# Kernel optimization log

Hardware: AMD Instinct MI355X
Metric: run time of the kernel (lower is better)

## Reference

```python
import jax, jax.numpy as jnp
import numpy as np

N_NODES = 10000
N_EDGES = 640000
F_IN = 128
F_HID = 128
BN_EPS = 1e-5


def _spectral_norm_weight(W, u):
    # One power iteration, matching torch.nn.utils.spectral_norm defaults.
    v = W.T @ u
    v = v / (jnp.linalg.norm(v) + 1e-12)
    u_new = W @ v
    u_new = u_new / (jnp.linalg.norm(u_new) + 1e-12)
    sigma = u_new @ (W @ v)
    return W / sigma


def setup_inputs() -> dict:
    key = jax.random.key(0)
    ks = jax.random.split(key, 8)
    x = jax.random.normal(ks[0], (N_NODES, F_IN), dtype=jnp.float32)
    edge_index = jax.random.randint(ks[1], (2, N_EDGES), 0, N_NODES, dtype=jnp.int64)
    W1 = jax.random.normal(ks[2], (F_HID, F_IN), dtype=jnp.float32) * (1.0 / np.sqrt(F_IN))
    b1 = jax.random.normal(ks[3], (F_HID,), dtype=jnp.float32) * 0.01
    u1 = jax.random.normal(ks[4], (F_HID,), dtype=jnp.float32)
    gamma = jnp.ones((F_HID,), dtype=jnp.float32)
    beta = jnp.zeros((F_HID,), dtype=jnp.float32)
    W2 = jax.random.normal(ks[5], (F_HID, F_HID), dtype=jnp.float32) * (1.0 / np.sqrt(F_HID))
    b2 = jax.random.normal(ks[6], (F_HID,), dtype=jnp.float32) * 0.01
    u2 = jax.random.normal(ks[7], (F_HID,), dtype=jnp.float32)
    return {"x": x, "edge_index": edge_index, "W1": W1, "b1": b1, "u1": u1,
            "gamma": gamma, "beta": beta, "W2": W2, "b2": b2, "u2": u2}


def reference(x, edge_index, W1, b1, u1, gamma, beta, W2, b2, u2):
    src, dst = edge_index[0], edge_index[1]
    # GINConv sum aggregation: out_i = sum_{j in N(i)} x_j
    agg = jax.ops.segment_sum(x[src], dst, num_segments=N_NODES)
    h = x + agg  # eps = 0 (default, train_eps=False)
    # MLP: SN-Linear -> ReLU -> BatchNorm1d (training stats) -> SN-Linear
    h = h @ _spectral_norm_weight(W1, u1).T + b1
    h = jax.nn.relu(h)
    mu = jnp.mean(h, axis=0)
    var = jnp.mean((h - mu) ** 2, axis=0)  # biased var, as torch BN forward
    h = gamma * (h - mu) / jnp.sqrt(var + BN_EPS) + beta
    h = h @ _spectral_norm_weight(W2, u2).T + b2
    return h
```

## Files before the change

kernel.cpp:

```cpp
#include <hip/hip_runtime.h>

#define NF 128
#define FB 128
#define CB 64
#define BPB 128
#define MAXNODE 10240

__device__ __forceinline__ unsigned short f2bf(float f) {
    unsigned int u = __float_as_uint(f);
    unsigned int r = u + 0x7FFFu + ((u >> 16) & 1u);
    return (unsigned short)(r >> 16);
}

__global__ __launch_bounds__(512) void power_hist_kernel(
    const float* __restrict__ W1, const float* __restrict__ u1,
    const float* __restrict__ W2, const float* __restrict__ u2,
    const int* __restrict__ dst, int n_edges,
    int* __restrict__ hist2d, int nbin,
    const float* __restrict__ x, unsigned short* __restrict__ xb, int n_x4,
    float* __restrict__ inv_sigma, float* __restrict__ W1t,
    float* __restrict__ colzero, int* __restrict__ cnts) {
    __shared__ float Wl[128][129];
    __shared__ float us[128], vv[128], part[4][128], red[128];
    __shared__ int hist[MAXNODE];
    int tid = threadIdx.x;

    if (blockIdx.x >= 2 + FB) {
        int cb = blockIdx.x - 2 - FB;
        const float4* x4 = (const float4*)x;
        ushort4* xb4 = (ushort4*)xb;
        for (int i = cb * 512 + tid; i < n_x4; i += CB * 512) {
            float4 v = x4[i];
            ushort4 o;
            o.x = f2bf(v.x); o.y = f2bf(v.y); o.z = f2bf(v.z); o.w = f2bf(v.w);
            xb4[i] = o;
        }
        return;
    }
    if (blockIdx.x >= 2) {
        int fb = blockIdx.x - 2;
        for (int i = tid; i < nbin; i += 512) hist[i] = 0;
        __syncthreads();
        int chunk = (n_edges + FB - 1) / FB;
        int e0 = fb * chunk, e1 = min(e0 + chunk, n_edges);
        int a0 = min(e1, (e0 + 3) & ~3);
        for (int e = e0 + tid; e < a0; e += 512) atomicAdd(&hist[dst[e]], 1);
        const int4* d4 = (const int4*)dst;
        int vs = a0 >> 2, ve = e1 >> 2;
        for (int i = vs + tid; i < ve; i += 512) {
            int4 d = d4[i];
            atomicAdd(&hist[d.x], 1);
            atomicAdd(&hist[d.y], 1);
            atomicAdd(&hist[d.z], 1);
            atomicAdd(&hist[d.w], 1);
        }
        for (int e = (ve << 2) + tid; e < e1; e += 512)
            if (e >= a0) atomicAdd(&hist[dst[e]], 1);
        __syncthreads();
        for (int i = tid; i < nbin; i += 512) hist2d[(size_t)fb * nbin + i] = hist[i];
        return;
    }

    const float* W = blockIdx.x ? W2 : W1;
    const float* u = blockIdx.x ? u2 : u1;
    const float4* W4 = (const float4*)W;
    for (int j = tid; j < 4096; j += 512) {
        float4 w = W4[j];
        int r = j >> 5, c0 = (j & 31) << 2;
        Wl[r][c0] = w.x; Wl[r][c0 + 1] = w.y; Wl[r][c0 + 2] = w.z; Wl[r][c0 + 3] = w.w;
    }
    if (tid < 128) us[tid] = u[tid];
    if (blockIdx.x == 0 && tid >= 256 && tid < 512) colzero[tid - 256] = 0.f;
    if (blockIdx.x == 0 && tid < 2) cnts[tid] = 0;
    __syncthreads();

    int c = tid & 127, sl = tid >> 7;
    float acc = 0.f;
#pragma unroll
    for (int j = 0; j < 32; ++j) acc = fmaf(Wl[sl * 32 + j][c], us[sl * 32 + j], acc);
    part[sl][c] = acc;
    __syncthreads();
    if (tid < 128) {
        float v = part[0][tid] + part[1][tid] + part[2][tid] + part[3][tid];
        vv[tid] = v;
        red[tid] = v * v;
    }
    __syncthreads();
    for (int s = 64; s > 0; s >>= 1) { if (tid < s) red[tid] += red[tid + s]; __syncthreads(); }
    float nv = sqrtf(red[0]) + 1e-12f;
    __syncthreads();
    if (tid < 128) vv[tid] = vv[tid] / nv;
    __syncthreads();

    float t = 0.f;
#pragma unroll
    for (int k = 0; k < 32; ++k) t = fmaf(Wl[c][sl * 32 + k], vv[sl * 32 + k], t);
    part[sl][c] = t;
    __syncthreads();
    if (tid < 128) {
        float tv = part[0][tid] + part[1][tid] + part[2][tid] + part[3][tid];
        red[tid] = tv * tv;
    }
    __syncthreads();
    for (int s = 64; s > 0; s >>= 1) { if (tid < s) red[tid] += red[tid + s]; __syncthreads(); }
    float tt = red[0];
    float is = (sqrtf(tt) + 1e-12f) / tt;
    if (tid == 0) inv_sigma[blockIdx.x] = is;
    if (blockIdx.x == 0) {
        for (int idx = tid; idx < 16384; idx += 512) {
            int k = idx >> 7, j = idx & 127;
            W1t[idx] = Wl[j][k] * is;
        }
    }
}

__global__ __launch_bounds__(512) void scanAB_kernel(int* __restrict__ hist2d,
                                                     int* __restrict__ binOff,
                                                     int nbin, int* __restrict__ cnt) {
    __shared__ int part[4][132];
    __shared__ int sbuf[MAXNODE];
    __shared__ int wsum2[8], wexcl2[8];
    __shared__ int isLast;
    int tid = threadIdx.x;
    int binrel = tid >> 2;
    int q = tid & 3;
    int bin = blockIdx.x * BPB + binrel;
    int fb0 = q * 32;

    int v[32];
    if (bin < nbin) {
#pragma unroll
        for (int f = 0; f < 32; ++f)
            v[f] = hist2d[(size_t)(fb0 + f) * nbin + bin];
        int partial = 0;
#pragma unroll
        for (int f = 0; f < 32; ++f) partial += v[f];
        part[q][binrel] = partial;
    }
    __syncthreads();
    if (bin < nbin) {
        int run = 0;
#pragma unroll
        for (int t = 0; t < 4; ++t)
            if (t < q) run += part[t][binrel];
#pragma unroll
        for (int f = 0; f < 32; ++f) {
            hist2d[(size_t)(fb0 + f) * nbin + bin] = run;
            run += v[f];
        }
        if (q == 3)
            binOff[bin] = part[0][binrel] + part[1][binrel] + part[2][binrel] + part[3][binrel];
    }

    __threadfence();
    __syncthreads();
    if (tid == 0) isLast = (atomicAdd(cnt, 1) == (int)gridDim.x - 1);
    __syncthreads();
    if (!isLast) return;
    __threadfence();

    for (int i = tid; i < nbin; i += 512) sbuf[i] = binOff[i];
    __syncthreads();
    int C = (nbin + 511) >> 9;
    int b0 = tid * C, b1 = min(b0 + C, nbin);
    int ssum = 0;
    for (int i = b0; i < b1; ++i) ssum += sbuf[i];
    int lane = tid & 63, wv = tid >> 6;
    int inc = ssum;
    for (int off = 1; off < 64; off <<= 1) {
        int t = __shfl_up(inc, off);
        if (lane >= off) inc += t;
    }
    if (lane == 63) wsum2[wv] = inc;
    __syncthreads();
    if (tid < 8) {
        int e2 = 0;
        for (int t = 0; t < 8; ++t)
            if (t < tid) e2 += wsum2[t];
        wexcl2[tid] = e2;
    }
    __syncthreads();
    int base = inc - ssum + wexcl2[wv];
    int run2 = base;
    for (int i = b0; i < b1; ++i) {
        int vv2 = sbuf[i];
        sbuf[i] = run2;
        run2 += vv2;
    }
    __syncthreads();
    for (int i = tid; i < nbin; i += 512) binOff[i] = sbuf[i];
    if (tid == 511) binOff[nbin] = wexcl2[7] + wsum2[7];
}

__global__ __launch_bounds__(512) void fill_kernel(
    const int* __restrict__ src, const int* __restrict__ dst,
    const int* __restrict__ hist2d, const int* __restrict__ binOff,
    int* __restrict__ bucket, int nbin, int n_edges) {
    __shared__ int cur[MAXNODE];
    int tid = threadIdx.x, fb = blockIdx.x;
    for (int i = tid; i < nbin; i += 512)
        cur[i] = hist2d[(size_t)fb * nbin + i] + binOff[i];
    __syncthreads();
    int chunk = (n_edges + FB - 1) / FB;
    int e0 = fb * chunk, e1 = min(e0 + chunk, n_edges);
    int a0 = min(e1, (e0 + 3) & ~3);
    for (int e = e0 + tid; e < a0; e += 512) {
        int pos = atomicAdd(&cur[dst[e]], 1);
        bucket[pos] = src[e];
    }
    const int4* d4 = (const int4*)dst;
    const int4* s4 = (const int4*)src;
    int vs = a0 >> 2, ve = e1 >> 2;
    for (int i = vs + tid; i < ve; i += 512) {
        int4 d = d4[i];
        int4 s = s4[i];
        int p0 = atomicAdd(&cur[d.x], 1);
        int p1 = atomicAdd(&cur[d.y], 1);
        int p2 = atomicAdd(&cur[d.z], 1);
        int p3 = atomicAdd(&cur[d.w], 1);
        bucket[p0] = s.x; bucket[p1] = s.y; bucket[p2] = s.z; bucket[p3] = s.w;
    }
    for (int e = (ve << 2) + tid; e < e1; e += 512)
        if (e >= a0) {
            int pos = atomicAdd(&cur[dst[e]], 1);
            bucket[pos] = src[e];
        }
}

__global__ __launch_bounds__(256) void gather_kernel(
    const unsigned short* __restrict__ xb, const int* __restrict__ bucket,
    const int* __restrict__ binOff, float* __restrict__ h0, int n_nodes) {
    int gw = (blockIdx.x * blockDim.x + threadIdx.x) >> 6;
    int lane = threadIdx.x & 63;
    if (gw >= n_nodes) return;
    const unsigned int* xu = (const unsigned int*)xb;
    unsigned int u0 = xu[(size_t)gw * 64 + lane];
    float2 acc;
    acc.x = __uint_as_float(u0 << 16);
    acc.y = __uint_as_float(u0 & 0xFFFF0000u);
    int j = binOff[gw], end = binOff[gw + 1];
    for (; j + 8 <= end; j += 8) {
        int s0 = bucket[j],     s1 = bucket[j + 1], s2 = bucket[j + 2], s3 = bucket[j + 3];
        int s4 = bucket[j + 4], s5 = bucket[j + 5], s6 = bucket[j + 6], s7 = bucket[j + 7];
        unsigned int v0 = xu[(size_t)s0 * 64 + lane];
        unsigned int v1 = xu[(size_t)s1 * 64 + lane];
        unsigned int v2 = xu[(size_t)s2 * 64 + lane];
        unsigned int v3 = xu[(size_t)s3 * 64 + lane];
        unsigned int v4 = xu[(size_t)s4 * 64 + lane];
        unsigned int v5 = xu[(size_t)s5 * 64 + lane];
        unsigned int v6 = xu[(size_t)s6 * 64 + lane];
        unsigned int v7 = xu[(size_t)s7 * 64 + lane];
        acc.x += __uint_as_float(v0 << 16) + __uint_as_float(v1 << 16)
               + __uint_as_float(v2 << 16) + __uint_as_float(v3 << 16)
               + __uint_as_float(v4 << 16) + __uint_as_float(v5 << 16)
               + __uint_as_float(v6 << 16) + __uint_as_float(v7 << 16);
        acc.y += __uint_as_float(v0 & 0xFFFF0000u) + __uint_as_float(v1 & 0xFFFF0000u)
               + __uint_as_float(v2 & 0xFFFF0000u) + __uint_as_float(v3 & 0xFFFF0000u)
               + __uint_as_float(v4 & 0xFFFF0000u) + __uint_as_float(v5 & 0xFFFF0000u)
               + __uint_as_float(v6 & 0xFFFF0000u) + __uint_as_float(v7 & 0xFFFF0000u);
    }
    for (; j < end; ++j) {
        unsigned int v = xu[(size_t)bucket[j] * 64 + lane];
        acc.x += __uint_as_float(v << 16);
        acc.y += __uint_as_float(v & 0xFFFF0000u);
    }
    ((float2*)h0)[(size_t)gw * 64 + lane] = acc;
}

__global__ void edge_scatter_kernel(const int* __restrict__ ei, const float* __restrict__ x,
                                    float* __restrict__ h0, int n_edges) {
    int gtid = blockIdx.x * blockDim.x + threadIdx.x;
    int wid = gtid >> 6;
    int lane = threadIdx.x & 63;
    int nw = (gridDim.x * blockDim.x) >> 6;
    const int* srcs = ei;
    const int* dsts = ei + n_edges;
    for (int e = wid; e < n_edges; e += nw) {
        int s = srcs[e];
        int d = dsts[e];
        atomicAdd(&h0[d * NF + lane], x[s * NF + lane]);
        atomicAdd(&h0[d * NF + 64 + lane], x[s * NF + 64 + lane]);
    }
}

template <bool RELU, bool BNACC>
__global__ __launch_bounds__(256, 4) void gemm16_kernel(
    const float* __restrict__ H, const float* __restrict__ Wt,
    const float* __restrict__ bias, float* __restrict__ O,
    float* __restrict__ colsum, float* __restrict__ colsumsq, int n_rows) {
    __shared__ float Hl[16][128];
    int tid = threadIdx.x;
    int m0 = blockIdx.x * 16;

    const float4* H4 = (const float4*)H;
    for (int j = tid; j < 512; j += 256) {
        int r = j >> 5, k4 = j & 31;
        int gr = m0 + r;
        float4 h = (gr < n_rows) ? H4[(size_t)gr * 32 + k4] : make_float4(0.f, 0.f, 0.f, 0.f);
        *(float4*)&Hl[r][k4 << 2] = h;
    }
    __syncthreads();

    int tx = tid & 31, ty = tid >> 5;
    int rb = ty * 2, cb = tx * 4;
    float acc[2][4] = {};
    const float4* Wt4 = (const float4*)Wt;

#pragma unroll 2
    for (int k = 0; k < 128; k += 4) {
        float4 w0 = Wt4[(k + 0) * 32 + tx];
        float4 w1 = Wt4[(k + 1) * 32 + tx];
        float4 w2 = Wt4[(k + 2) * 32 + tx];
        float4 w3 = Wt4[(k + 3) * 32 + tx];
        float wv[4][4] = {{w0.x, w0.y, w0.z, w0.w}, {w1.x, w1.y, w1.z, w1.w},
                          {w2.x, w2.y, w2.z, w2.w}, {w3.x, w3.y, w3.z, w3.w}};
#pragma unroll
        for (int i = 0; i < 2; ++i) {
            float4 h = *(const float4*)&Hl[rb + i][k];
            float hf[4] = {h.x, h.y, h.z, h.w};
#pragma unroll
            for (int kk = 0; kk < 4; ++kk)
#pragma unroll
                for (int j = 0; j < 4; ++j)
                    acc[i][j] = fmaf(hf[kk], wv[kk][j], acc[i][j]);
        }
    }

    float bv[4];
#pragma unroll
    for (int j = 0; j < 4; ++j) bv[j] = bias[cb + j];

    float s[4] = {0.f, 0.f, 0.f, 0.f}, q[4] = {0.f, 0.f, 0.f, 0.f};
#pragma unroll
    for (int i = 0; i < 2; ++i) {
        int gr = m0 + rb + i;
        if (gr < n_rows) {
            float o[4];
#pragma unroll
            for (int j = 0; j < 4; ++j) {
                float v = acc[i][j] + bv[j];
                if (RELU) v = fmaxf(v, 0.f);
                o[j] = v;
                if (BNACC) { s[j] += v; q[j] = fmaf(v, v, q[j]); }
            }
            *(float4*)&O[(size_t)gr * NF + cb] = make_float4(o[0], o[1], o[2], o[3]);
        }
    }

    if (BNACC) {
        __syncthreads();
        float* sS = &Hl[0][0];
        float* sQ = &Hl[8][0];
#pragma unroll
        for (int j = 0; j < 4; ++j) {
            sS[ty * 128 + cb + j] = s[j];
            sQ[ty * 128 + cb + j] = q[j];
        }
        __syncthreads();
        if (tid < 128) {
            float ts = 0.f, tq = 0.f;
#pragma unroll
            for (int g = 0; g < 8; ++g) {
                ts += sS[g * 128 + tid];
                tq += sQ[g * 128 + tid];
            }
            atomicAdd(&colsum[tid], ts);
            atomicAdd(&colsumsq[tid], tq);
        }
    }
}

__global__ void fold_kernel(const float* __restrict__ W2, const float* __restrict__ b2,
                            const float* __restrict__ gamma, const float* __restrict__ beta,
                            const float* __restrict__ colsum, const float* __restrict__ colsumsq,
                            const float* __restrict__ inv_sigma, float* __restrict__ W2pt,
                            float* __restrict__ b2p, float inv_n) {
    __shared__ float a[128], cc[128], red[128];
    int k = threadIdx.x;
    int j = blockIdx.x;
    float mu = colsum[k] * inv_n;
    float var = colsumsq[k] * inv_n - mu * mu;
    float ai = gamma[k] / sqrtf(var + 1e-5f);
    a[k] = ai;
    cc[k] = beta[k] - ai * mu;
    __syncthreads();
    float is2 = inv_sigma[1];
    float wv = W2[j * 128 + k] * is2;
    W2pt[k * 128 + j] = wv * a[k];
    red[k] = wv * cc[k];
    __syncthreads();
    for (int s = 64; s > 0; s >>= 1) { if (k < s) red[k] += red[k + s]; __syncthreads(); }
    if (k == 0) b2p[j] = b2[j] + red[0];
}

extern "C" void kernel_launch(void* const* d_in, const int* in_sizes, int n_in,
                              void* d_out, int out_size, void* d_ws, size_t ws_size,
                              hipStream_t stream) {
    const float* x     = (const float*)d_in[0];
    const int*   ei    = (const int*)d_in[1];
    const float* W1    = (const float*)d_in[2];
    const float* b1    = (const float*)d_in[3];
    const float* u1    = (const float*)d_in[4];
    const float* gamma = (const float*)d_in[5];
    const float* beta  = (const float*)d_in[6];
    const float* W2    = (const float*)d_in[7];
    const float* b2    = (const float*)d_in[8];
    const float* u2    = (const float*)d_in[9];
    float* out = (float*)d_out;

    int n_nodes = in_sizes[0] / NF;
    int n_edges = in_sizes[1] / 2;
    int nbin = n_nodes;
    int nbin_pad = (nbin + 1 + 3) & ~3;
    int nedge_pad = (n_edges + 3) & ~3;
    size_t scratch = (size_t)FB * nbin > (size_t)n_nodes * NF
                   ? (size_t)FB * nbin : (size_t)n_nodes * NF;
    scratch = (scratch + 3) & ~(size_t)3;

    float* ws        = (float*)d_ws;
    float* inv_sigma = ws;
    float* colsum    = ws + 4;
    float* colsumsq  = colsum + 128;
    float* W1t       = colsumsq + 128;
    float* W2pt      = W1t + 16384;
    float* b2p       = W2pt + 16384;
    int*   cnts      = (int*)(b2p + 128);
    int*   binOff    = cnts + 4;
    int*   bucket    = binOff + nbin_pad;
    int*   hist2d    = bucket + nedge_pad;
    float* h0        = (float*)hist2d;
    unsigned short* xb = (unsigned short*)(hist2d + scratch);
    float* h0g       = (float*)(xb + (size_t)n_nodes * NF);

    size_t need = (size_t)(33160 + nbin_pad + nedge_pad + scratch) * 4
                + (size_t)n_nodes * NF * 2 + (size_t)n_nodes * NF * 4;
    bool fused = (n_nodes <= MAXNODE) && (ws_size >= need);

    int n_x4 = n_nodes * 32;
    int gemm_blocks = (n_nodes + 15) / 16;

    if (fused) {
        power_hist_kernel<<<2 + FB + CB, 512, 0, stream>>>(
            W1, u1, W2, u2, ei + n_edges, n_edges, hist2d, nbin,
            x, xb, n_x4, inv_sigma, W1t, colsum, cnts);
        scanAB_kernel<<<(nbin + BPB - 1) / BPB, 512, 0, stream>>>(hist2d, binOff, nbin,
                                                                  &cnts[0]);
        fill_kernel<<<FB, 512, 0, stream>>>(ei, ei + n_edges, hist2d, binOff, bucket,
                                            nbin, n_edges);
        gather_kernel<<<(n_nodes * 64 + 255) / 256, 256, 0, stream>>>(
            xb, bucket, binOff, h0g, n_nodes);
        gemm16_kernel<true, true><<<gemm_blocks, 256, 0, stream>>>(
            h0g, W1t, b1, out, colsum, colsumsq, n_nodes);
    } else {
        power_hist_kernel<<<2, 512, 0, stream>>>(
            W1, u1, W2, u2, ei + n_edges, n_edges, hist2d, nbin,
            x, xb, 0, inv_sigma, W1t, colsum, cnts);
        hipMemcpyAsync(h0, x, (size_t)n_nodes * NF * sizeof(float),
                       hipMemcpyDeviceToDevice, stream);
        edge_scatter_kernel<<<2048, 256, 0, stream>>>(ei, x, h0, n_edges);
        gemm16_kernel<true, true><<<gemm_blocks, 256, 0, stream>>>(
            h0, W1t, b1, out, colsum, colsumsq, n_nodes);
    }

    fold_kernel<<<128, 128, 0, stream>>>(W2, b2, gamma, beta, colsum, colsumsq,
                                         inv_sigma, W2pt, b2p, 1.0f / (float)n_nodes);

    gemm16_kernel<false, false><<<gemm_blocks, 256, 0, stream>>>(
        out, W2pt, b2p, out, nullptr, nullptr, n_nodes);
}
```

Baseline: 123.6 us.

## Fuse BN fold into first GEMM via last-block pattern; store weights as bf16

The separate fold kernel is removed on the fused path. The last block of the first GEMM, found with an atomic counter, computes the BatchNorm scale and shift and writes the folded W2 and bias. Both weight matrices are now stored as bf16 and unpacked in the GEMM inner loop, halving weight-load bandwidth. This saves one launch but lowers weight precision, and the fold runs serially in a single block at the tail of the first GEMM.

```diff
diff --git a/kernel.cpp b/kernel.cpp
--- a/kernel.cpp
+++ b/kernel.cpp
@@ -11,6 +11,8 @@
     unsigned int r = u + 0x7FFFu + ((u >> 16) & 1u);
     return (unsigned short)(r >> 16);
 }
+__device__ __forceinline__ float bfl(unsigned int u) { return __uint_as_float(u << 16); }
+__device__ __forceinline__ float bfh(unsigned int u) { return __uint_as_float(u & 0xFFFF0000u); }
 
 __global__ __launch_bounds__(512) void power_hist_kernel(
     const float* __restrict__ W1, const float* __restrict__ u1,
@@ -18,7 +20,7 @@
     const int* __restrict__ dst, int n_edges,
     int* __restrict__ hist2d, int nbin,
     const float* __restrict__ x, unsigned short* __restrict__ xb, int n_x4,
-    float* __restrict__ inv_sigma, float* __restrict__ W1t,
+    float* __restrict__ inv_sigma, unsigned short* __restrict__ W1tb,
     float* __restrict__ colzero, int* __restrict__ cnts) {
     __shared__ float Wl[128][129];
     __shared__ float us[128], vv[128], part[4][128], red[128];
@@ -109,7 +111,7 @@
     if (blockIdx.x == 0) {
         for (int idx = tid; idx < 16384; idx += 512) {
             int k = idx >> 7, j = idx & 127;
-            W1t[idx] = Wl[j][k] * is;
+            W1tb[idx] = f2bf(Wl[j][k] * is);
         }
     }
 }
@@ -236,8 +238,8 @@
     const unsigned int* xu = (const unsigned int*)xb;
     unsigned int u0 = xu[(size_t)gw * 64 + lane];
     float2 acc;
-    acc.x = __uint_as_float(u0 << 16);
-    acc.y = __uint_as_float(u0 & 0xFFFF0000u);
+    acc.x = bfl(u0);
+    acc.y = bfh(u0);
     int j = binOff[gw], end = binOff[gw + 1];
     for (; j + 8 <= end; j += 8) {
         int s0 = bucket[j],     s1 = bucket[j + 1], s2 = bucket[j + 2], s3 = bucket[j + 3];
@@ -250,19 +252,13 @@
         unsigned int v5 = xu[(size_t)s5 * 64 + lane];
         unsigned int v6 = xu[(size_t)s6 * 64 + lane];
         unsigned int v7 = xu[(size_t)s7 * 64 + lane];
-        acc.x += __uint_as_float(v0 << 16) + __uint_as_float(v1 << 16)
-               + __uint_as_float(v2 << 16) + __uint_as_float(v3 << 16)
-               + __uint_as_float(v4 << 16) + __uint_as_float(v5 << 16)
-               + __uint_as_float(v6 << 16) + __uint_as_float(v7 << 16);
-        acc.y += __uint_as_float(v0 & 0xFFFF0000u) + __uint_as_float(v1 & 0xFFFF0000u)
-               + __uint_as_float(v2 & 0xFFFF0000u) + __uint_as_float(v3 & 0xFFFF0000u)
-               + __uint_as_float(v4 & 0xFFFF0000u) + __uint_as_float(v5 & 0xFFFF0000u)
-               + __uint_as_float(v6 & 0xFFFF0000u) + __uint_as_float(v7 & 0xFFFF0000u);
+        acc.x += bfl(v0) + bfl(v1) + bfl(v2) + bfl(v3) + bfl(v4) + bfl(v5) + bfl(v6) + bfl(v7);
+        acc.y += bfh(v0) + bfh(v1) + bfh(v2) + bfh(v3) + bfh(v4) + bfh(v5) + bfh(v6) + bfh(v7);
     }
     for (; j < end; ++j) {
         unsigned int v = xu[(size_t)bucket[j] * 64 + lane];
-        acc.x += __uint_as_float(v << 16);
-        acc.y += __uint_as_float(v & 0xFFFF0000u);
+        acc.x += bfl(v);
+        acc.y += bfh(v);
     }
     ((float2*)h0)[(size_t)gw * 64 + lane] = acc;
 }
@@ -283,11 +279,15 @@
     }
 }
 
-template <bool RELU, bool BNACC>
+template <bool RELU, bool BNACC, bool FOLD>
 __global__ __launch_bounds__(256, 4) void gemm16_kernel(
-    const float* __restrict__ H, const float* __restrict__ Wt,
+    const float* __restrict__ H, const unsigned short* __restrict__ Wt,
     const float* __restrict__ bias, float* __restrict__ O,
-    float* __restrict__ colsum, float* __restrict__ colsumsq, int n_rows) {
+    float* __restrict__ colsum, float* __restrict__ colsumsq, int n_rows,
+    const float* __restrict__ W2, const float* __restrict__ b2,
+    const float* __restrict__ gamma, const float* __restrict__ beta,
+    const float* __restrict__ inv_sigma, unsigned short* __restrict__ W2ptb,
+    float* __restrict__ b2p, int* __restrict__ cnt, float inv_n) {
     __shared__ float Hl[16][128];
     int tid = threadIdx.x;
     int m0 = blockIdx.x * 16;
@@ -304,16 +304,18 @@
     int tx = tid & 31, ty = tid >> 5;
     int rb = ty * 2, cb = tx * 4;
     float acc[2][4] = {};
-    const float4* Wt4 = (const float4*)Wt;
+    const uint2* Wb = (const uint2*)Wt;
 
 #pragma unroll 2
     for (int k = 0; k < 128; k += 4) {
-        float4 w0 = Wt4[(k + 0) * 32 + tx];
-        float4 w1 = Wt4[(k + 1) * 32 + tx];
-        float4 w2 = Wt4[(k + 2) * 32 + tx];
-        float4 w3 = Wt4[(k + 3) * 32 + tx];
-        float wv[4][4] = {{w0.x, w0.y, w0.z, w0.w}, {w1.x, w1.y, w1.z, w1.w},
-                          {w2.x, w2.y, w2.z, w2.w}, {w3.x, w3.y, w3.z, w3.w}};
+        uint2 u0 = Wb[(k + 0) * 32 + tx];
+        uint2 u1 = Wb[(k + 1) * 32 + tx];
+        uint2 u2 = Wb[(k + 2) * 32 + tx];
+        uint2 u3 = Wb[(k + 3) * 32 + tx];
+        float wv[4][4] = {{bfl(u0.x), bfh(u0.x), bfl(u0.y), bfh(u0.y)},
+                          {bfl(u1.x), bfh(u1.x), bfl(u1.y), bfh(u1.y)},
+                          {bfl(u2.x), bfh(u2.x), bfl(u2.y), bfh(u2.y)},
+                          {bfl(u3.x), bfh(u3.x), bfl(u3.y), bfh(u3.y)}};
 #pragma unroll
         for (int i = 0; i < 2; ++i) {
             float4 h = *(const float4*)&Hl[rb + i][k];
@@ -368,12 +370,49 @@
             atomicAdd(&colsumsq[tid], tq);
         }
     }
+
+    if (FOLD) {
+        __threadfence();
+        __syncthreads();
+        __shared__ int isLast;
+        if (tid == 0) isLast = (atomicAdd(cnt, 1) == (int)gridDim.x - 1);
+        __syncthreads();
+        if (!isLast) return;
+        __threadfence();
+
+        __shared__ float a_s[128], c_s[128], bred[256];
+        if (tid < 128) {
+            float mu = colsum[tid] * inv_n;
+            float var = colsumsq[tid] * inv_n - mu * mu;
+            float ai = gamma[tid] / sqrtf(var + 1e-5f);
+            a_s[tid] = ai;
+            c_s[tid] = beta[tid] - ai * mu;
+        }
+        __syncthreads();
+        float is2 = inv_sigma[0];
+        int j = tid & 127, half = tid >> 7;
+        const float4* W24 = (const float4*)W2;
+        float bacc = 0.f;
+        for (int k4 = half * 16; k4 < half * 16 + 16; ++k4) {
+            float4 w = W24[j * 32 + k4];
+            int k = k4 << 2;
+            w.x *= is2; w.y *= is2; w.z *= is2; w.w *= is2;
+            W2ptb[(k + 0) * 128 + j] = f2bf(w.x * a_s[k + 0]);
+            W2ptb[(k + 1) * 128 + j] = f2bf(w.y * a_s[k + 1]);
+            W2ptb[(k + 2) * 128 + j] = f2bf(w.z * a_s[k + 2]);
+            W2ptb[(k + 3) * 128 + j] = f2bf(w.w * a_s[k + 3]);
+            bacc += w.x * c_s[k] + w.y * c_s[k + 1] + w.z * c_s[k + 2] + w.w * c_s[k + 3];
+        }
+        bred[tid] = bacc;
+        __syncthreads();
+        if (tid < 128) b2p[tid] = b2[tid] + bred[tid] + bred[tid + 128];
+    }
 }
 
 __global__ void fold_kernel(const float* __restrict__ W2, const float* __restrict__ b2,
                             const float* __restrict__ gamma, const float* __restrict__ beta,
                             const float* __restrict__ colsum, const float* __restrict__ colsumsq,
-                            const float* __restrict__ inv_sigma, float* __restrict__ W2pt,
+                            const float* __restrict__ inv_sigma, unsigned short* __restrict__ W2ptb,
                             float* __restrict__ b2p, float inv_n) {
     __shared__ float a[128], cc[128], red[128];
     int k = threadIdx.x;
@@ -386,7 +425,7 @@
     __syncthreads();
     float is2 = inv_sigma[1];
     float wv = W2[j * 128 + k] * is2;
-    W2pt[k * 128 + j] = wv * a[k];
+    W2ptb[k * 128 + j] = f2bf(wv * a[k]);
     red[k] = wv * cc[k];
     __syncthreads();
     for (int s = 64; s > 0; s >>= 1) { if (k < s) red[k] += red[k + s]; __syncthreads(); }
@@ -421,18 +460,18 @@
     float* inv_sigma = ws;
     float* colsum    = ws + 4;
     float* colsumsq  = colsum + 128;
-    float* W1t       = colsumsq + 128;
-    float* W2pt      = W1t + 16384;
-    float* b2p       = W2pt + 16384;
-    int*   cnts      = (int*)(b2p + 128);
-    int*   binOff    = cnts + 4;
+    float* b2p       = colsumsq + 128;
+    unsigned short* W1tb  = (unsigned short*)(ws + 388);
+    unsigned short* W2ptb = (unsigned short*)(ws + 8580);
+    int*   cnts      = (int*)(ws + 16772);
+    int*   binOff    = (int*)(ws + 16776);
     int*   bucket    = binOff + nbin_pad;
     int*   hist2d    = bucket + nedge_pad;
     float* h0        = (float*)hist2d;
     unsigned short* xb = (unsigned short*)(hist2d + scratch);
     float* h0g       = (float*)(xb + (size_t)n_nodes * NF);
 
-    size_t need = (size_t)(33160 + nbin_pad + nedge_pad + scratch) * 4
+    size_t need = (size_t)(16776 + nbin_pad + nedge_pad + scratch) * 4
                 + (size_t)n_nodes * NF * 2 + (size_t)n_nodes * NF * 4;
     bool fused = (n_nodes <= MAXNODE) && (ws_size >= need);
 
@@ -442,29 +481,32 @@
     if (fused) {
         power_hist_kernel<<<2 + FB + CB, 512, 0, stream>>>(
             W1, u1, W2, u2, ei + n_edges, n_edges, hist2d, nbin,
-            x, xb, n_x4, inv_sigma, W1t, colsum, cnts);
+            x, xb, n_x4, inv_sigma, W1tb, colsum, cnts);
         scanAB_kernel<<<(nbin + BPB - 1) / BPB, 512, 0, stream>>>(hist2d, binOff, nbin,
                                                                   &cnts[0]);
         fill_kernel<<<FB, 512, 0, stream>>>(ei, ei + n_edges, hist2d, binOff, bucket,
                                             nbin, n_edges);
         gather_kernel<<<(n_nodes * 64 + 255) / 256, 256, 0, stream>>>(
             xb, bucket, binOff, h0g, n_nodes);
-        gemm16_kernel<true, true><<<gemm_blocks, 256, 0, stream>>>(
-            h0g, W1t, b1, out, colsum, colsumsq, n_nodes);
+        gemm16_kernel<true, true, true><<<gemm_blocks, 256, 0, stream>>>(
+            h0g, W1tb, b1, out, colsum, colsumsq, n_nodes,
+            W2, b2, gamma, beta, inv_sigma + 1, W2ptb, b2p, &cnts[1],
+            1.0f / (float)n_nodes);
     } else {
         power_hist_kernel<<<2, 512, 0, stream>>>(
             W1, u1, W2, u2, ei + n_edges, n_edges, hist2d, nbin,
-            x, xb, 0, inv_sigma, W1t, colsum, cnts);
+            x, xb, 0, inv_sigma, W1tb, colsum, cnts);
         hipMemcpyAsync(h0, x, (size_t)n_nodes * NF * sizeof(float),
                        hipMemcpyDeviceToDevice, stream);
         edge_scatter_kernel<<<2048, 256, 0, stream>>>(ei, x, h0, n_edges);
-        gemm16_kernel<true, true><<<gemm_blocks, 256, 0, stream>>>(
-            h0, W1t, b1, out, colsum, colsumsq, n_nodes);
-    }
-
-    fold_kernel<<<128, 128, 0, stream>>>(W2, b2, gamma, beta, colsum, colsumsq,
-                                         inv_sigma, W2pt, b2p, 1.0f / (float)n_nodes);
-
-    gemm16_kernel<false, false><<<gemm_blocks, 256, 0, stream>>>(
-        out, W2pt, b2p, out, nullptr, nullptr, n_nodes);
-}
+        gemm16_kernel<true, true, false><<<gemm_blocks, 256, 0, stream>>>(
+            h0, W1tb, b1, out, colsum, colsumsq, n_nodes,
+            nullptr, nullptr, nullptr, nullptr, nullptr, nullptr, nullptr, nullptr, 0.f);
+        fold_kernel<<<128, 128, 0, stream>>>(W2, b2, gamma, beta, colsum, colsumsq,
+                                             inv_sigma, W2ptb, b2p, 1.0f / (float)n_nodes);
+    }
+
+    gemm16_kernel<false, false, false><<<gemm_blocks, 256, 0, stream>>>(
+        out, W2ptb, b2p, out, nullptr, nullptr, n_nodes,
+        nullptr, nullptr, nullptr, nullptr, nullptr, nullptr, nullptr, nullptr, 0.f);
+}
```

Measured after the change: 152.2 us. +23.1%, slower.
